# Optimization experiments

Hardware: AMD Instinct MI355X
Metric: run time of the kernel (lower is better)

Reference implementation:

```python
import jax, jax.numpy as jnp
import numpy as np

NUM_STEPS = 10
T0, T1 = 0.0, 1.0


def setup_inputs() -> dict:
    key = jax.random.key(0)
    ks = jax.random.split(key, 6)
    B, I, H = 4096, 1024, 2048
    sc_ih = 1.0 / np.sqrt(I)
    sc_hh = 1.0 / np.sqrt(H)
    return {
        "x": jax.random.normal(ks[0], (B, I), jnp.float32),
        "h0": jax.random.normal(ks[1], (B, H), jnp.float32),
        "W_ih": jax.random.normal(ks[2], (H, I), jnp.float32) * sc_ih,
        "b_ih": jax.random.normal(ks[3], (H,), jnp.float32) * sc_ih,
        "W_hh": jax.random.normal(ks[4], (H, H), jnp.float32) * sc_hh,
        "b_hh": jax.random.normal(ks[5], (H,), jnp.float32) * sc_hh,
        "tau": jnp.ones((H,), jnp.float32),
    }


def reference(x, h0, W_ih, b_ih, W_hh, b_hh, tau):
    dt = (T1 - T0) / NUM_STEPS
    # time-invariant input drive: W_ih(input) is the same every step
    ih = x @ W_ih.T + b_ih  # [B, H]
    decay = jnp.exp(-dt / tau)  # [H]

    def step(h, _):
        pre = ih + h @ W_hh.T + b_hh
        target = jnp.tanh(pre)
        h_new = decay * h + (1.0 - decay) * target
        return h_new, None

    h_final, _ = jax.lax.scan(step, h0, None, length=NUM_STEPS)
    return h_final
```

## Files before the change

kernel.cpp:

```cpp
#include <hip/hip_runtime.h>
#include <hip/hip_bf16.h>

#define NUM_STEPS 10
#define DT 0.1f
#define SLOT_BYTES 49152

typedef __bf16 bf16_t;
typedef __bf16 bf16x8 __attribute__((ext_vector_type(8)));
typedef __bf16 bf16x4 __attribute__((ext_vector_type(4)));
typedef float f32x4 __attribute__((ext_vector_type(4)));

__device__ __forceinline__ void async16(const bf16_t* g, bf16_t* l) {
  __builtin_amdgcn_global_load_lds(
      (const __attribute__((address_space(1))) void*)g,
      (__attribute__((address_space(3))) void*)l, 16, 0, 0);
}

__global__ void cvt_f32_to_bf16(const float* __restrict__ in,
                                bf16_t* __restrict__ out, int n4) {
  int i = blockIdx.x * blockDim.x + threadIdx.x;
  if (i < n4) {
    float4 v = ((const float4*)in)[i];
    bf16x4 o = {(bf16_t)v.x, (bf16_t)v.y, (bf16_t)v.z, (bf16_t)v.w};
    ((bf16x4*)out)[i] = o;
  }
}

__global__ void make_decay(const float* __restrict__ tau,
                           float* __restrict__ decay, int n) {
  int i = blockIdx.x * blockDim.x + threadIdx.x;
  if (i < n) decay[i] = __expf(-DT / tau[i]);
}

template <int EPI>
__global__ __launch_bounds__(512, 2) void gemm_nt(
    const bf16_t* __restrict__ A, const bf16_t* __restrict__ Bw, int M, int N,
    int K, const float* __restrict__ bias1, const float* __restrict__ bias2,
    bf16_t* __restrict__ out_ihb, const bf16_t* __restrict__ ihb,
    const float* __restrict__ decay, const bf16_t* __restrict__ hb_prev,
    bf16_t* __restrict__ hb_next, float* __restrict__ out_f32, int writeOut) {
  extern __shared__ char smem[];

  const int tid = threadIdx.x;
  const int lane = tid & 63;
  const int wave = tid >> 6;
  const int waveM = wave >> 1;
  const int waveN = wave & 1;

  const int lin = blockIdx.y * gridDim.x + blockIdx.x;
  const int xcd = lin & 7;
  const int slot_ = lin >> 3;
  const int bx = (xcd & 1) * 8 + (slot_ & 7);
  const int by = (xcd >> 1) * 4 + (slot_ >> 3);
  const long bRow = (long)by * 256;
  const long bCol = (long)bx * 128;

  const int laneRow = lane & 15;
  const int laneK = (lane >> 4) << 3;
  const bf16_t* aGlo = A + (bRow + wave * 16 + laneRow) * (long)K + laneK;
  const bf16_t* aGhi = A + (bRow + 128 + wave * 16 + laneRow) * (long)K + laneK;
  const bf16_t* bG = Bw + (bCol + wave * 16 + laneRow) * (long)K + laneK;

  f32x4 acc[4][4] = {};

  auto stageA = [&](int slot, int k0) {
    bf16_t* base = (bf16_t*)(smem + slot * SLOT_BYTES);
    async16(aGlo + k0, base + wave * 1024);
    async16(aGlo + k0 + 32, base + wave * 1024 + 512);
    async16(aGhi + k0, base + (8 + wave) * 1024);
    async16(aGhi + k0 + 32, base + (8 + wave) * 1024 + 512);
  };
  auto stageB = [&](int slot, int k0) {
    bf16_t* base = (bf16_t*)(smem + slot * SLOT_BYTES);
    async16(bG + k0, base + 16384 + wave * 1024);
    async16(bG + k0 + 32, base + 16384 + wave * 1024 + 512);
  };

  const int NT = K >> 6;

  stageA(0, 0);
  stageB(0, 0);
  stageA(1, 64);
  stageB(1, 64);
  asm volatile("s_waitcnt vmcnt(6)" ::: "memory");
  __builtin_amdgcn_s_barrier();
  __builtin_amdgcn_sched_barrier(0);

  for (int t = 0; t < NT; ++t) {
    const int slot = t % 3;
    const int ns = (t + 2) % 3;
    const int k2 = (t + 2) * 64;
    const bool pf = (t + 2) < NT;
    const bf16_t* Ab = (const bf16_t*)(smem + slot * SLOT_BYTES);
    const bf16_t* Bb = Ab + 16384;

    {
      bf16x8 aF[4], bF[4];
#pragma unroll
      for (int i = 0; i < 4; ++i)
        aF[i] = *(const bf16x8*)&Ab[(waveM * 4 + i) * 1024 + lane * 8];
#pragma unroll
      for (int u = 0; u < 4; ++u)
        bF[u] = *(const bf16x8*)&Bb[(waveN * 4 + u) * 1024 + lane * 8];
      if (pf) stageA(ns, k2);
      __builtin_amdgcn_sched_barrier(0);
      __builtin_amdgcn_s_barrier();
      __builtin_amdgcn_s_setprio(1);
#pragma unroll
      for (int i = 0; i < 4; ++i)
#pragma unroll
        for (int u = 0; u < 4; ++u)
          acc[i][u] = __builtin_amdgcn_mfma_f32_16x16x32_bf16(
              aF[i], bF[u], acc[i][u], 0, 0, 0);
      __builtin_amdgcn_s_setprio(0);
      __builtin_amdgcn_sched_barrier(0);
      __builtin_amdgcn_s_barrier();
    }
    {
      bf16x8 aF[4], bF[4];
#pragma unroll
      for (int i = 0; i < 4; ++i)
        aF[i] = *(const bf16x8*)&Ab[(waveM * 4 + i) * 1024 + 512 + lane * 8];
#pragma unroll
      for (int u = 0; u < 4; ++u)
        bF[u] = *(const bf16x8*)&Bb[(waveN * 4 + u) * 1024 + 512 + lane * 8];
      if (pf) stageB(ns, k2);
      __builtin_amdgcn_sched_barrier(0);
      __builtin_amdgcn_s_barrier();
      __builtin_amdgcn_s_setprio(1);
#pragma unroll
      for (int i = 0; i < 4; ++i)
#pragma unroll
        for (int u = 0; u < 4; ++u)
          acc[i][u] = __builtin_amdgcn_mfma_f32_16x16x32_bf16(
              aF[i], bF[u], acc[i][u], 0, 0, 0);
      __builtin_amdgcn_s_setprio(0);
      if (t < NT - 2) {
        asm volatile("s_waitcnt vmcnt(6)" ::: "memory");
      } else if (t == NT - 2) {
        asm volatile("s_waitcnt vmcnt(0)" ::: "memory");
      }
      __builtin_amdgcn_sched_barrier(0);
      __builtin_amdgcn_s_barrier();
    }
  }

  float* Ep = (float*)smem;
  const int eRow = (lane >> 4) << 2;
  const int eCol = lane & 15;
#pragma unroll
  for (int i = 0; i < 4; ++i)
#pragma unroll
    for (int u = 0; u < 4; ++u)
#pragma unroll
      for (int r = 0; r < 4; ++r) {
        const int rowL = waveM * 64 + i * 16 + eRow + r;
        const int colL = waveN * 64 + u * 16 + eCol;
        Ep[rowL * 128 + ((colL + 4 * rowL) & 127)] = acc[i][u][r];
      }
  asm volatile("s_waitcnt lgkmcnt(0)" ::: "memory");
  __builtin_amdgcn_s_barrier();
  __builtin_amdgcn_sched_barrier(0);

  const int rdRow = tid >> 3;
  const int col0 = (tid & 7) * 16;
#pragma unroll
  for (int p = 0; p < 4; ++p) {
    const int row = p * 64 + rdRow;
    float v[16];
#pragma unroll
    for (int c = 0; c < 4; ++c)
      *(f32x4*)&v[c * 4] =
          *(const f32x4*)&Ep[row * 128 + ((col0 + 4 * c + 4 * row) & 127)];
    const long g = (bRow + row) * (long)N + bCol + col0;

    if (EPI == 0) {
      f32x4 b1[4], b2[4];
#pragma unroll
      for (int c = 0; c < 4; ++c) {
        b1[c] = *(const f32x4*)&bias1[bCol + col0 + c * 4];
        b2[c] = *(const f32x4*)&bias2[bCol + col0 + c * 4];
      }
      bf16x8 o0, o1;
#pragma unroll
      for (int e = 0; e < 8; ++e)
        o0[e] = (bf16_t)(v[e] + b1[e >> 2][e & 3] + b2[e >> 2][e & 3]);
#pragma unroll
      for (int e = 0; e < 8; ++e)
        o1[e] = (bf16_t)(v[8 + e] + b1[2 + (e >> 2)][e & 3] +
                         b2[2 + (e >> 2)][e & 3]);
      *(bf16x8*)&out_ihb[g] = o0;
      *(bf16x8*)&out_ihb[g + 8] = o1;
    } else {
      const bf16x8 ih0 = *(const bf16x8*)&ihb[g];
      const bf16x8 ih1 = *(const bf16x8*)&ihb[g + 8];
      const bf16x8 hp0 = *(const bf16x8*)&hb_prev[g];
      const bf16x8 hp1 = *(const bf16x8*)&hb_prev[g + 8];
      f32x4 dc[4];
#pragma unroll
      for (int c = 0; c < 4; ++c)
        dc[c] = *(const f32x4*)&decay[bCol + col0 + c * 4];
      float hn[16];
      bf16x8 o0, o1;
#pragma unroll
      for (int e = 0; e < 8; ++e) {
        const float d = dc[e >> 2][e & 3];
        const float th = tanhf(v[e] + (float)ih0[e]);
        hn[e] = d * (float)hp0[e] + (1.0f - d) * th;
        o0[e] = (bf16_t)hn[e];
      }
#pragma unroll
      for (int e = 0; e < 8; ++e) {
        const float d = dc[2 + (e >> 2)][e & 3];
        const float th = tanhf(v[8 + e] + (float)ih1[e]);
        hn[8 + e] = d * (float)hp1[e] + (1.0f - d) * th;
        o1[e] = (bf16_t)hn[8 + e];
      }
      *(bf16x8*)&hb_next[g] = o0;
      *(bf16x8*)&hb_next[g + 8] = o1;
      if (writeOut) {
#pragma unroll
        for (int c = 0; c < 4; ++c)
          *(f32x4*)&out_f32[g + c * 4] = *(const f32x4*)&hn[c * 4];
      }
    }
  }
}

extern "C" void kernel_launch(void* const* d_in, const int* in_sizes, int n_in,
                              void* d_out, int out_size, void* d_ws,
                              size_t ws_size, hipStream_t stream) {
  const float* x = (const float*)d_in[0];
  const float* h0 = (const float*)d_in[1];
  const float* W_ih = (const float*)d_in[2];
  const float* b_ih = (const float*)d_in[3];
  const float* W_hh = (const float*)d_in[4];
  const float* b_hh = (const float*)d_in[5];
  const float* tau = (const float*)d_in[6];
  float* hout = (float*)d_out;

  const int B = 4096, I = 1024, H = 2048;

  char* ws = (char*)d_ws;
  bf16_t* ihb = (bf16_t*)ws; ws += (size_t)B * H * 2;
  bf16_t* hb0 = (bf16_t*)ws; ws += (size_t)B * H * 2;
  bf16_t* hb1 = (bf16_t*)ws; ws += (size_t)B * H * 2;
  bf16_t* xb = (bf16_t*)ws;  ws += (size_t)B * I * 2;
  bf16_t* wihb = (bf16_t*)ws; ws += (size_t)H * I * 2;
  bf16_t* whhb = (bf16_t*)ws; ws += (size_t)H * H * 2;
  float* decay = (float*)ws; ws += (size_t)H * 4;

  const int LDS_BYTES = 147456;
  (void)hipFuncSetAttribute(reinterpret_cast<const void*>(&gemm_nt<0>),
                            hipFuncAttributeMaxDynamicSharedMemorySize,
                            LDS_BYTES);
  (void)hipFuncSetAttribute(reinterpret_cast<const void*>(&gemm_nt<1>),
                            hipFuncAttributeMaxDynamicSharedMemorySize,
                            LDS_BYTES);

  cvt_f32_to_bf16<<<(B * I / 4 + 255) / 256, 256, 0, stream>>>(x, xb, B * I / 4);
  cvt_f32_to_bf16<<<(H * I / 4 + 255) / 256, 256, 0, stream>>>(W_ih, wihb, H * I / 4);
  cvt_f32_to_bf16<<<(H * H / 4 + 255) / 256, 256, 0, stream>>>(W_hh, whhb, H * H / 4);
  cvt_f32_to_bf16<<<(B * H / 4 + 255) / 256, 256, 0, stream>>>(h0, hb0, B * H / 4);
  make_decay<<<(H + 255) / 256, 256, 0, stream>>>(tau, decay, H);

  dim3 grid(H / 128, B / 256);
  gemm_nt<0><<<grid, 512, LDS_BYTES, stream>>>(
      xb, wihb, B, H, I, b_ih, b_hh, ihb, nullptr, nullptr, nullptr, nullptr,
      nullptr, 0);

  bf16_t* hb[2] = {hb0, hb1};
  for (int s = 0; s < NUM_STEPS; ++s) {
    gemm_nt<1><<<grid, 512, LDS_BYTES, stream>>>(
        hb[s & 1], whhb, B, H, H, nullptr, nullptr, nullptr, ihb, decay,
        hb[s & 1], hb[(s + 1) & 1], hout, (s == NUM_STEPS - 1) ? 1 : 0);
  }
}
```

Baseline: 739.8 us.

## Enlarge GEMM block tile to 256x256 with double-buffered LDS pipeline

Block tile grows from 256x128 to 256x256, with 8 waves arranged 2x4, each wave computing a 128x64 sub-tile (acc[8][4]). The LDS pipeline changes from triple buffering to double buffering with 64KB slots, split into four half-step phases that interleave A/B prefetch with MFMA groups. The epilogue is staged through LDS in two halves. The intent is more MFMA work per LDS byte and higher arithmetic intensity. The trade-offs are a grid of only 128 blocks for 256 CUs, more accumulator registers, and a shallower prefetch depth.

```diff
diff --git a/kernel.cpp b/kernel.cpp
--- a/kernel.cpp
+++ b/kernel.cpp
@@ -3,7 +3,6 @@
 
 #define NUM_STEPS 10
 #define DT 0.1f
-#define SLOT_BYTES 49152
 
 typedef __bf16 bf16_t;
 typedef __bf16 bf16x8 __attribute__((ext_vector_type(8)));
@@ -44,184 +43,224 @@
   const int tid = threadIdx.x;
   const int lane = tid & 63;
   const int wave = tid >> 6;
-  const int waveM = wave >> 1;
-  const int waveN = wave & 1;
+  const int waveM = wave >> 2;
+  const int waveN = wave & 3;
 
   const int lin = blockIdx.y * gridDim.x + blockIdx.x;
   const int xcd = lin & 7;
   const int slot_ = lin >> 3;
-  const int bx = (xcd & 1) * 8 + (slot_ & 7);
-  const int by = (xcd >> 1) * 4 + (slot_ >> 3);
+  const int bx = (xcd & 1) * 4 + (slot_ & 3);
+  const int by = (xcd >> 1) * 4 + (slot_ >> 2);
   const long bRow = (long)by * 256;
-  const long bCol = (long)bx * 128;
+  const long bCol = (long)bx * 256;
 
   const int laneRow = lane & 15;
   const int laneK = (lane >> 4) << 3;
   const bf16_t* aGlo = A + (bRow + wave * 16 + laneRow) * (long)K + laneK;
-  const bf16_t* aGhi = A + (bRow + 128 + wave * 16 + laneRow) * (long)K + laneK;
-  const bf16_t* bG = Bw + (bCol + wave * 16 + laneRow) * (long)K + laneK;
-
-  f32x4 acc[4][4] = {};
-
-  auto stageA = [&](int slot, int k0) {
-    bf16_t* base = (bf16_t*)(smem + slot * SLOT_BYTES);
-    async16(aGlo + k0, base + wave * 1024);
-    async16(aGlo + k0 + 32, base + wave * 1024 + 512);
-    async16(aGhi + k0, base + (8 + wave) * 1024);
-    async16(aGhi + k0 + 32, base + (8 + wave) * 1024 + 512);
+  const bf16_t* aGhi = A + (bRow + (8 + wave) * 16 + laneRow) * (long)K + laneK;
+  const bf16_t* bGlo = Bw + (bCol + wave * 16 + laneRow) * (long)K + laneK;
+  const bf16_t* bGhi = Bw + (bCol + (8 + wave) * 16 + laneRow) * (long)K + laneK;
+
+  f32x4 acc[8][4] = {};
+
+  auto uA = [&](int buf, int k0, int ks) {
+    bf16_t* base = (bf16_t*)(smem + buf * 65536);
+    async16(aGlo + k0 + ks * 32, base + wave * 1024 + ks * 512);
+    async16(aGhi + k0 + ks * 32, base + (8 + wave) * 1024 + ks * 512);
   };
-  auto stageB = [&](int slot, int k0) {
-    bf16_t* base = (bf16_t*)(smem + slot * SLOT_BYTES);
-    async16(bG + k0, base + 16384 + wave * 1024);
-    async16(bG + k0 + 32, base + 16384 + wave * 1024 + 512);
+  auto uB = [&](int buf, int k0, int ks) {
+    bf16_t* base = (bf16_t*)(smem + buf * 65536);
+    async16(bGlo + k0 + ks * 32, base + 16384 + wave * 1024 + ks * 512);
+    async16(bGhi + k0 + ks * 32, base + 16384 + (8 + wave) * 1024 + ks * 512);
   };
 
   const int NT = K >> 6;
 
-  stageA(0, 0);
-  stageB(0, 0);
-  stageA(1, 64);
-  stageB(1, 64);
-  asm volatile("s_waitcnt vmcnt(6)" ::: "memory");
+  uA(0, 0, 0);
+  uB(0, 0, 0);
+  uA(0, 0, 1);
+  uB(0, 0, 1);
+  asm volatile("s_waitcnt vmcnt(4)" ::: "memory");
   __builtin_amdgcn_s_barrier();
   __builtin_amdgcn_sched_barrier(0);
 
   for (int t = 0; t < NT; ++t) {
-    const int slot = t % 3;
-    const int ns = (t + 2) % 3;
-    const int k2 = (t + 2) * 64;
-    const bool pf = (t + 2) < NT;
-    const bf16_t* Ab = (const bf16_t*)(smem + slot * SLOT_BYTES);
+    const int cur = t & 1, nxt = cur ^ 1;
+    const int k1 = (t + 1) << 6;
+    const bool pf = (t + 1) < NT;
+    const bf16_t* Ab = (const bf16_t*)(smem + cur * 65536);
     const bf16_t* Bb = Ab + 16384;
-
-    {
-      bf16x8 aF[4], bF[4];
-#pragma unroll
-      for (int i = 0; i < 4; ++i)
-        aF[i] = *(const bf16x8*)&Ab[(waveM * 4 + i) * 1024 + lane * 8];
+    bf16x8 aF[4], bF[4];
+
+#pragma unroll
+    for (int i = 0; i < 4; ++i)
+      aF[i] = *(const bf16x8*)&Ab[(waveM * 8 + i) * 1024 + lane * 8];
+#pragma unroll
+    for (int u = 0; u < 4; ++u)
+      bF[u] = *(const bf16x8*)&Bb[(waveN * 4 + u) * 1024 + lane * 8];
+    if (pf) uA(nxt, k1, 0);
+    __builtin_amdgcn_s_barrier();
+    asm volatile("s_waitcnt lgkmcnt(0)" ::: "memory");
+    __builtin_amdgcn_sched_barrier(0);
+    __builtin_amdgcn_s_setprio(1);
+#pragma unroll
+    for (int i = 0; i < 4; ++i)
 #pragma unroll
       for (int u = 0; u < 4; ++u)
-        bF[u] = *(const bf16x8*)&Bb[(waveN * 4 + u) * 1024 + lane * 8];
-      if (pf) stageA(ns, k2);
-      __builtin_amdgcn_sched_barrier(0);
-      __builtin_amdgcn_s_barrier();
-      __builtin_amdgcn_s_setprio(1);
-#pragma unroll
-      for (int i = 0; i < 4; ++i)
-#pragma unroll
-        for (int u = 0; u < 4; ++u)
-          acc[i][u] = __builtin_amdgcn_mfma_f32_16x16x32_bf16(
-              aF[i], bF[u], acc[i][u], 0, 0, 0);
-      __builtin_amdgcn_s_setprio(0);
-      __builtin_amdgcn_sched_barrier(0);
-      __builtin_amdgcn_s_barrier();
+        acc[i][u] = __builtin_amdgcn_mfma_f32_16x16x32_bf16(aF[i], bF[u],
+                                                            acc[i][u], 0, 0, 0);
+    __builtin_amdgcn_s_setprio(0);
+    __builtin_amdgcn_sched_barrier(0);
+    __builtin_amdgcn_s_barrier();
+
+#pragma unroll
+    for (int i = 0; i < 4; ++i)
+      aF[i] = *(const bf16x8*)&Ab[(waveM * 8 + 4 + i) * 1024 + lane * 8];
+    if (pf) uB(nxt, k1, 0);
+    __builtin_amdgcn_s_barrier();
+    asm volatile("s_waitcnt lgkmcnt(0)" ::: "memory");
+    __builtin_amdgcn_sched_barrier(0);
+    __builtin_amdgcn_s_setprio(1);
+#pragma unroll
+    for (int i = 0; i < 4; ++i)
+#pragma unroll
+      for (int u = 0; u < 4; ++u)
+        acc[4 + i][u] = __builtin_amdgcn_mfma_f32_16x16x32_bf16(
+            aF[i], bF[u], acc[4 + i][u], 0, 0, 0);
+    __builtin_amdgcn_s_setprio(0);
+    if (t < NT - 1) {
+      asm volatile("s_waitcnt vmcnt(4)" ::: "memory");
+    } else {
+      asm volatile("s_waitcnt vmcnt(0)" ::: "memory");
     }
-    {
-      bf16x8 aF[4], bF[4];
-#pragma unroll
-      for (int i = 0; i < 4; ++i)
-        aF[i] = *(const bf16x8*)&Ab[(waveM * 4 + i) * 1024 + 512 + lane * 8];
+    __builtin_amdgcn_sched_barrier(0);
+    __builtin_amdgcn_s_barrier();
+
+#pragma unroll
+    for (int i = 0; i < 4; ++i)
+      aF[i] = *(const bf16x8*)&Ab[(waveM * 8 + i) * 1024 + 512 + lane * 8];
+#pragma unroll
+    for (int u = 0; u < 4; ++u)
+      bF[u] = *(const bf16x8*)&Bb[(waveN * 4 + u) * 1024 + 512 + lane * 8];
+    if (pf) uA(nxt, k1, 1);
+    __builtin_amdgcn_s_barrier();
+    asm volatile("s_waitcnt lgkmcnt(0)" ::: "memory");
+    __builtin_amdgcn_sched_barrier(0);
+    __builtin_amdgcn_s_setprio(1);
+#pragma unroll
+    for (int i = 0; i < 4; ++i)
 #pragma unroll
       for (int u = 0; u < 4; ++u)
-        bF[u] = *(const bf16x8*)&Bb[(waveN * 4 + u) * 1024 + 512 + lane * 8];
-      if (pf) stageB(ns, k2);
-      __builtin_amdgcn_sched_barrier(0);
-      __builtin_amdgcn_s_barrier();
-      __builtin_amdgcn_s_setprio(1);
-#pragma unroll
-      for (int i = 0; i < 4; ++i)
-#pragma unroll
-        for (int u = 0; u < 4; ++u)
-          acc[i][u] = __builtin_amdgcn_mfma_f32_16x16x32_bf16(
-              aF[i], bF[u], acc[i][u], 0, 0, 0);
-      __builtin_amdgcn_s_setprio(0);
-      if (t < NT - 2) {
-        asm volatile("s_waitcnt vmcnt(6)" ::: "memory");
-      } else if (t == NT - 2) {
-        asm volatile("s_waitcnt vmcnt(0)" ::: "memory");
-      }
-      __builtin_amdgcn_sched_barrier(0);
-      __builtin_amdgcn_s_barrier();
+        acc[i][u] = __builtin_amdgcn_mfma_f32_16x16x32_bf16(aF[i], bF[u],
+                                                            acc[i][u], 0, 0, 0);
+    __builtin_amdgcn_s_setprio(0);
+    __builtin_amdgcn_sched_barrier(0);
+    __builtin_amdgcn_s_barrier();
+
+#pragma unroll
+    for (int i = 0; i < 4; ++i)
+      aF[i] = *(const bf16x8*)&Ab[(waveM * 8 + 4 + i) * 1024 + 512 + lane * 8];
+    if (pf) uB(nxt, k1, 1);
+    __builtin_amdgcn_s_barrier();
+    asm volatile("s_waitcnt lgkmcnt(0)" ::: "memory");
+    __builtin_amdgcn_sched_barrier(0);
+    __builtin_amdgcn_s_setprio(1);
+#pragma unroll
+    for (int i = 0; i < 4; ++i)
+#pragma unroll
+      for (int u = 0; u < 4; ++u)
+        acc[4 + i][u] = __builtin_amdgcn_mfma_f32_16x16x32_bf16(
+            aF[i], bF[u], acc[4 + i][u], 0, 0, 0);
+    __builtin_amdgcn_s_setprio(0);
+    if (t < NT - 1) {
+      asm volatile("s_waitcnt vmcnt(4)" ::: "memory");
     }
+    __builtin_amdgcn_sched_barrier(0);
+    __builtin_amdgcn_s_barrier();
   }
 
   float* Ep = (float*)smem;
   const int eRow = (lane >> 4) << 2;
   const int eCol = lane & 15;
-#pragma unroll
-  for (int i = 0; i < 4; ++i)
-#pragma unroll
-    for (int u = 0; u < 4; ++u)
-#pragma unroll
-      for (int r = 0; r < 4; ++r) {
-        const int rowL = waveM * 64 + i * 16 + eRow + r;
-        const int colL = waveN * 64 + u * 16 + eCol;
-        Ep[rowL * 128 + ((colL + 4 * rowL) & 127)] = acc[i][u][r];
-      }
-  asm volatile("s_waitcnt lgkmcnt(0)" ::: "memory");
-  __builtin_amdgcn_s_barrier();
-  __builtin_amdgcn_sched_barrier(0);
-
-  const int rdRow = tid >> 3;
-  const int col0 = (tid & 7) * 16;
-#pragma unroll
-  for (int p = 0; p < 4; ++p) {
-    const int row = p * 64 + rdRow;
-    float v[16];
-#pragma unroll
-    for (int c = 0; c < 4; ++c)
-      *(f32x4*)&v[c * 4] =
-          *(const f32x4*)&Ep[row * 128 + ((col0 + 4 * c + 4 * row) & 127)];
-    const long g = (bRow + row) * (long)N + bCol + col0;
-
-    if (EPI == 0) {
-      f32x4 b1[4], b2[4];
-#pragma unroll
-      for (int c = 0; c < 4; ++c) {
-        b1[c] = *(const f32x4*)&bias1[bCol + col0 + c * 4];
-        b2[c] = *(const f32x4*)&bias2[bCol + col0 + c * 4];
-      }
-      bf16x8 o0, o1;
-#pragma unroll
-      for (int e = 0; e < 8; ++e)
-        o0[e] = (bf16_t)(v[e] + b1[e >> 2][e & 3] + b2[e >> 2][e & 3]);
-#pragma unroll
-      for (int e = 0; e < 8; ++e)
-        o1[e] = (bf16_t)(v[8 + e] + b1[2 + (e >> 2)][e & 3] +
-                         b2[2 + (e >> 2)][e & 3]);
-      *(bf16x8*)&out_ihb[g] = o0;
-      *(bf16x8*)&out_ihb[g + 8] = o1;
-    } else {
-      const bf16x8 ih0 = *(const bf16x8*)&ihb[g];
-      const bf16x8 ih1 = *(const bf16x8*)&ihb[g + 8];
-      const bf16x8 hp0 = *(const bf16x8*)&hb_prev[g];
-      const bf16x8 hp1 = *(const bf16x8*)&hb_prev[g + 8];
-      f32x4 dc[4];
+  const int rdRow = tid >> 2;
+  const int rq = tid & 3;
+
+  for (int p = 0; p < 2; ++p) {
+    if (p) __syncthreads();
+    if (waveM == p) {
+#pragma unroll
+      for (int rf = 0; rf < 8; ++rf)
+#pragma unroll
+        for (int cf = 0; cf < 4; ++cf)
+#pragma unroll
+          for (int r = 0; r < 4; ++r) {
+            const int rowL = rf * 16 + eRow + r;
+            const int colL = waveN * 64 + cf * 16 + eCol;
+            Ep[rowL * 256 + ((colL + 4 * rowL) & 255)] = acc[rf][cf][r];
+          }
+    }
+    __syncthreads();
+
+    const long grow = bRow + p * 128 + rdRow;
+#pragma unroll
+    for (int c4 = 0; c4 < 4; ++c4) {
+      const int col0 = rq * 16 + c4 * 64;
+      float v[16];
 #pragma unroll
       for (int c = 0; c < 4; ++c)
-        dc[c] = *(const f32x4*)&decay[bCol + col0 + c * 4];
-      float hn[16];
-      bf16x8 o0, o1;
-#pragma unroll
-      for (int e = 0; e < 8; ++e) {
-        const float d = dc[e >> 2][e & 3];
-        const float th = tanhf(v[e] + (float)ih0[e]);
-        hn[e] = d * (float)hp0[e] + (1.0f - d) * th;
-        o0[e] = (bf16_t)hn[e];
-      }
-#pragma unroll
-      for (int e = 0; e < 8; ++e) {
-        const float d = dc[2 + (e >> 2)][e & 3];
-        const float th = tanhf(v[8 + e] + (float)ih1[e]);
-        hn[8 + e] = d * (float)hp1[e] + (1.0f - d) * th;
-        o1[e] = (bf16_t)hn[8 + e];
-      }
-      *(bf16x8*)&hb_next[g] = o0;
-      *(bf16x8*)&hb_next[g + 8] = o1;
-      if (writeOut) {
+        *(f32x4*)&v[c * 4] =
+            *(const f32x4*)&Ep[rdRow * 256 + ((col0 + 4 * c + 4 * rdRow) & 255)];
+      const long g = grow * (long)N + bCol + col0;
+
+      if (EPI == 0) {
+        f32x4 b1[4], b2[4];
+#pragma unroll
+        for (int c = 0; c < 4; ++c) {
+          b1[c] = *(const f32x4*)&bias1[bCol + col0 + c * 4];
+          b2[c] = *(const f32x4*)&bias2[bCol + col0 + c * 4];
+        }
+        bf16x8 o0, o1;
+#pragma unroll
+        for (int e = 0; e < 8; ++e)
+          o0[e] = (bf16_t)(v[e] + b1[e >> 2][e & 3] + b2[e >> 2][e & 3]);
+#pragma unroll
+        for (int e = 0; e < 8; ++e)
+          o1[e] = (bf16_t)(v[8 + e] + b1[2 + (e >> 2)][e & 3] +
+                           b2[2 + (e >> 2)][e & 3]);
+        *(bf16x8*)&out_ihb[g] = o0;
+        *(bf16x8*)&out_ihb[g + 8] = o1;
+      } else {
+        const bf16x8 ih0 = *(const bf16x8*)&ihb[g];
+        const bf16x8 ih1 = *(const bf16x8*)&ihb[g + 8];
+        const bf16x8 hp0 = *(const bf16x8*)&hb_prev[g];
+        const bf16x8 hp1 = *(const bf16x8*)&hb_prev[g + 8];
+        f32x4 dc[4];
 #pragma unroll
         for (int c = 0; c < 4; ++c)
-          *(f32x4*)&out_f32[g + c * 4] = *(const f32x4*)&hn[c * 4];
+          dc[c] = *(const f32x4*)&decay[bCol + col0 + c * 4];
+        float hn[16];
+        bf16x8 o0, o1;
+#pragma unroll
+        for (int e = 0; e < 8; ++e) {
+          const float d = dc[e >> 2][e & 3];
+          const float th = tanhf(v[e] + (float)ih0[e]);
+          hn[e] = d * (float)hp0[e] + (1.0f - d) * th;
+          o0[e] = (bf16_t)hn[e];
+        }
+#pragma unroll
+        for (int e = 0; e < 8; ++e) {
+          const float d = dc[2 + (e >> 2)][e & 3];
+          const float th = tanhf(v[8 + e] + (float)ih1[e]);
+          hn[8 + e] = d * (float)hp1[e] + (1.0f - d) * th;
+          o1[e] = (bf16_t)hn[8 + e];
+        }
+        *(bf16x8*)&hb_next[g] = o0;
+        *(bf16x8*)&hb_next[g + 8] = o1;
+        if (writeOut) {
+#pragma unroll
+          for (int c = 0; c < 4; ++c)
+            *(f32x4*)&out_f32[g + c * 4] = *(const f32x4*)&hn[c * 4];
+        }
       }
     }
   }
@@ -250,7 +289,7 @@
   bf16_t* whhb = (bf16_t*)ws; ws += (size_t)H * H * 2;
   float* decay = (float*)ws; ws += (size_t)H * 4;
 
-  const int LDS_BYTES = 147456;
+  const int LDS_BYTES = 131072;
   (void)hipFuncSetAttribute(reinterpret_cast<const void*>(&gemm_nt<0>),
                             hipFuncAttributeMaxDynamicSharedMemorySize,
                             LDS_BYTES);
@@ -264,7 +303,7 @@
   cvt_f32_to_bf16<<<(B * H / 4 + 255) / 256, 256, 0, stream>>>(h0, hb0, B * H / 4);
   make_decay<<<(H + 255) / 256, 256, 0, stream>>>(tau, decay, H);
 
-  dim3 grid(H / 128, B / 256);
+  dim3 grid(H / 256, B / 256);
   gemm_nt<0><<<grid, 512, LDS_BYTES, stream>>>(
       xb, wihb, B, H, I, b_ih, b_hh, ihb, nullptr, nullptr, nullptr, nullptr,
       nullptr, 0);
```

New measurement: 1.994 ms. +169.5%, slower.
